# Kernel tuning notes

Measured on AMD Instinct MI355X. Metric: run time of the kernel, lower is better.

## Reference

```python
import jax, jax.numpy as jnp
import numpy as np

DECAY = 0.999
EPS = 1e-05
COMMITMENT_COST = 0.25
M, D = 1024, 256
B, H, W = 32, 32, 32


def setup_inputs() -> dict:
    key = jax.random.key(0)
    k1, k2 = jax.random.split(key)
    init_bound = 1.0 / M
    x = jax.random.normal(k1, (B, H, W, D), dtype=jnp.float32)
    embedding = jax.random.uniform(k2, (M, D), dtype=jnp.float32,
                                   minval=-init_bound, maxval=init_bound)
    ema_count = jnp.zeros((M,), dtype=jnp.float32)
    ema_weight = embedding  # buffer initialized as embedding.clone()
    return {"x": x, "embedding": embedding, "ema_count": ema_count,
            "ema_weight": ema_weight}


def reference(x, embedding, ema_count, ema_weight):
    Mn, Dn = embedding.shape
    x_flat = jax.lax.stop_gradient(x).reshape(-1, Dn)          # [N, D]
    N = x_flat.shape[0]

    # (-cdist)^2 == squared euclidean distance; argmin is the same.
    x_sq = jnp.sum(x_flat * x_flat, axis=-1, keepdims=True)    # [N, 1]
    e_sq = jnp.sum(embedding * embedding, axis=-1)             # [M]
    distances = x_sq - 2.0 * (x_flat @ embedding.T) + e_sq[None, :]  # [N, M]
    indices = jnp.argmin(distances, axis=-1)                   # [N]

    quantized = embedding[indices].reshape(x.shape)            # gather

    # one-hot column sums == scatter-add of ones; encodings.T @ x_flat == scatter-add rows
    counts = jnp.zeros((Mn,), x.dtype).at[indices].add(1.0)    # [M]
    dw = jnp.zeros((Mn, Dn), x.dtype).at[indices].add(x_flat)  # [M, D]

    new_count = DECAY * ema_count + (1.0 - DECAY) * counts
    n = jnp.sum(new_count)
    new_count = (new_count + EPS) / (n + Mn * EPS) * n
    new_weight = DECAY * ema_weight + (1.0 - DECAY) * dw
    new_embedding = new_weight / new_count[:, None]

    codebook_loss = jnp.mean((jax.lax.stop_gradient(x) - quantized) ** 2)
    e_latent_loss = jnp.mean((x - jax.lax.stop_gradient(quantized)) ** 2)
    commitment_loss = COMMITMENT_COST * e_latent_loss

    quantized_st = x + jax.lax.stop_gradient(quantized - x)    # straight-through

    avg_probs = counts / N
    perplexity = jnp.exp(-jnp.sum(avg_probs * jnp.log(avg_probs + 1e-10)))

    return (quantized_st, commitment_loss, codebook_loss, perplexity,
            new_embedding, new_count, new_weight)
```

## Files before the change

kernel.cpp:

```cpp
#include <hip/hip_runtime.h>
#include <cfloat>
#include <math.h>

#define N_TOK 32768
#define DIM   256
#define MCODE 1024

typedef unsigned short u16;
typedef unsigned long long u64;
typedef __attribute__((ext_vector_type(8))) _Float16 h16x8;
typedef __attribute__((ext_vector_type(4))) float f32x4;

constexpr float DECAY_ = 0.999f;
constexpr float OMD_   = (float)(1.0 - 0.999);
constexpr float EPS_   = 1e-5f;
constexpr float MEPS_  = (float)(1024 * 1e-5);

constexpr int WS_EH   = 0;
constexpr int WS_EL   = 131072;
constexpr int WS_ESQ  = 262144;
constexpr int WS_CNTI = 263168;
constexpr int WS_BI   = 264192;
constexpr int WS_LP   = 296960;
constexpr int WS_KEY  = 299008;

constexpr int OUT_Q        = 0;
constexpr int OUT_COMMIT   = 8388608;
constexpr int OUT_CODEBOOK = 8388609;
constexpr int OUT_PERP     = 8388610;
constexpr int OUT_NE       = 8388611;
constexpr int OUT_NC       = 8650755;
constexpr int OUT_NW       = 8651779;

static __device__ __forceinline__ void gl2lds16(const u16* g, char* l) {
    __builtin_amdgcn_global_load_lds(
        (const __attribute__((address_space(1))) unsigned int*)g,
        (__attribute__((address_space(3))) unsigned int*)l, 16, 0, 0);
}
static __device__ __forceinline__ unsigned fmap(float f) {
    unsigned u = __float_as_uint(f);
    return (u & 0x80000000u) ? ~u : (u | 0x80000000u);
}

static __device__ __forceinline__ void load_row8(const float* __restrict__ src,
                                                 int wave_id, int lane,
                                                 float* vv, size_t* o) {
    int rb = wave_id >> 6, kc = (wave_id >> 3) & 7, t = wave_id & 7;
    int row = rb * 128 + t * 16 + (lane & 15);
    int k   = kc * 32 + (lane >> 4) * 8;
    const float* s = &src[row * DIM + k];
    float4 v0 = *(const float4*)s, v1 = *(const float4*)(s + 4);
    vv[0]=v0.x; vv[1]=v0.y; vv[2]=v0.z; vv[3]=v0.w;
    vv[4]=v1.x; vv[5]=v1.y; vv[6]=v1.z; vv[7]=v1.w;
    *o = (size_t)wave_id * 512 + lane * 8;
}
static __device__ __forceinline__ void pack_wave_h16(const float* __restrict__ src,
                                                     u16* __restrict__ dst,
                                                     int wave_id, int lane,
                                                     float scale) {
    float vv[8]; size_t o;
    load_row8(src, wave_id, lane, vv, &o);
    h16x8 hv;
#pragma unroll
    for (int j = 0; j < 8; ++j) hv[j] = (_Float16)(vv[j] * scale);
    *(h16x8*)&dst[o] = hv;
}

__global__ __launch_bounds__(256) void vq_setup(const float* __restrict__ x,
                                                const float* __restrict__ emb,
                                                u16* __restrict__ xh,
                                                u16* __restrict__ eh,
                                                float* __restrict__ esq,
                                                u64* __restrict__ keys,
                                                int* __restrict__ cnti) {
    const int b = blockIdx.x, tid = threadIdx.x;
    const int lane = tid & 63, w = tid >> 6;
    if (b < 4096) { pack_wave_h16(x, xh, b * 4 + w, lane, 1.0f); return; }
    const int p = b - 4096;
    if (p < 128) {
        pack_wave_h16(emb, eh, p * 4 + w, lane, 1024.0f);
    } else if (p < 384) {
        int c = (p - 128) * 4 + w;
        float4 v = *(const float4*)&emb[c * DIM + lane * 4];
        float s = v.x * v.x + v.y * v.y + v.z * v.z + v.w * v.w;
#pragma unroll
        for (int off = 32; off; off >>= 1) s += __shfl_xor(s, off, 64);
        if (lane == 0) esq[c] = s;
    } else if (p < 512) {
        keys[(p - 384) * 256 + tid] = ~0ULL;
    } else {
#pragma unroll
        for (int i = 0; i < 4; ++i) cnti[i * 256 + tid] = 0;
    }
}

__global__ __launch_bounds__(256) void vq_scores_mfma(const u16* __restrict__ xh,
                                                      const u16* __restrict__ eh,
                                                      const float* __restrict__ esq,
                                                      u64* __restrict__ keys) {
    __shared__ __align__(16) char smem[33792];
    const int tid  = threadIdx.x;
    const int lane = tid & 63, w = tid >> 6;
    const int wm = w & 1, wn = w >> 1;
    const int raw = blockIdx.x;
    const int rb = (raw >> 6) * 8 + (raw & 7);
    const int cs = (raw >> 3) & 7;

    const u16* gb0 = xh + (size_t)rb * 32768;
    const u16* gb1 = eh + (size_t)cs * 32768;

    const h16x8* Ah = (const h16x8*)(smem);
    const h16x8* Bh = (const h16x8*)(smem + 8192);

    f32x4 acc[4][4];
#pragma unroll
    for (int i = 0; i < 4; ++i)
#pragma unroll
        for (int j = 0; j < 4; ++j) acc[i][j] = (f32x4)0.f;

    for (int kc = 0; kc < 8; ++kc) {
        __syncthreads();
#pragma unroll
        for (int j = 0; j < 4; ++j) {
            int t = w * 4 + j;
            int arr = t >> 3, slot = t & 7;
            const u16* g = (arr == 0 ? gb0 : gb1)
                           + kc * 4096 + slot * 512 + lane * 8;
            gl2lds16(g, smem + arr * 8192 + slot * 1024);
        }
        __syncthreads();

        h16x8 ah[4];
#pragma unroll
        for (int tm = 0; tm < 4; ++tm)
            ah[tm] = Ah[(wm * 4 + tm) * 64 + lane];
#pragma unroll
        for (int tn = 0; tn < 4; ++tn) {
            h16x8 bh = Bh[(wn * 4 + tn) * 64 + lane];
#pragma unroll
            for (int tm = 0; tm < 4; ++tm) {
                acc[tm][tn] = __builtin_amdgcn_mfma_f32_16x16x32_f16(ah[tm], bh, acc[tm][tn], 0, 0, 0);
            }
        }
    }

    __syncthreads();
    float* cv = (float*)smem;
    int*   ci = (int*)(smem + 16896);
    const int ln = lane & 15, quad = lane >> 4;
#pragma unroll
    for (int tm = 0; tm < 4; ++tm) {
        float bv[4];
        int   bi[4];
#pragma unroll
        for (int r = 0; r < 4; ++r) { bv[r] = FLT_MAX; bi[r] = 0; }
#pragma unroll
        for (int tn = 0; tn < 4; ++tn) {
            int c = cs * 128 + wn * 64 + tn * 16 + ln;
            float ec = esq[c];
#pragma unroll
            for (int r = 0; r < 4; ++r) {
                float d = fmaf(-0.001953125f, acc[tm][tn][r], ec);
                if (d < bv[r]) { bv[r] = d; bi[r] = c; }
            }
        }
        int row0 = wm * 64 + tm * 16 + quad * 4;
        int slot = wn * 16 + ln;
#pragma unroll
        for (int r = 0; r < 4; ++r) {
            cv[(row0 + r) * 33 + slot] = bv[r];
            ci[(row0 + r) * 33 + slot] = bi[r];
        }
    }
    __syncthreads();
    if (tid < 128) {
        float bv = cv[tid * 33];
        int   bi = ci[tid * 33];
#pragma unroll
        for (int s = 1; s < 32; ++s) {
            float v = cv[tid * 33 + s];
            int  ix = ci[tid * 33 + s];
            if (v < bv || (v == bv && ix < bi)) { bv = v; bi = ix; }
        }
        u64 key = ((u64)fmap(bv) << 32) | (unsigned)bi;
        atomicMin(&keys[rb * 128 + tid], key);
    }
}

__global__ __launch_bounds__(256) void vq_quant(const float* __restrict__ x,
                                                const float* __restrict__ emb,
                                                const u64* __restrict__ keys,
                                                float* __restrict__ outq,
                                                int* __restrict__ cnti,
                                                int* __restrict__ bi_arr,
                                                float* __restrict__ lpart) {
    const int tid = threadIdx.x, lane = tid & 63, w = tid >> 6;
    const float4* x4 = (const float4*)x;
    const float4* e4 = (const float4*)emb;
    float4* o4 = (float4*)outq;
    float lacc = 0.f;
#pragma unroll
    for (int it = 0; it < 4; ++it) {
        int row = blockIdx.x * 16 + it * 4 + w;
        int bi = (int)(unsigned)(keys[row] & 0xffffffffULL);
        if (lane == 0) { atomicAdd(&cnti[bi], 1); bi_arr[row] = bi; }
        float4 xv = x4[row * 64 + lane];
        float4 ev = e4[bi * 64 + lane];
        float4 q;
        q.x = xv.x + (ev.x - xv.x);  q.y = xv.y + (ev.y - xv.y);
        q.z = xv.z + (ev.z - xv.z);  q.w = xv.w + (ev.w - xv.w);
        o4[row * 64 + lane] = q;
        float dx = xv.x - ev.x, dy = xv.y - ev.y, dz = xv.z - ev.z, dwv = xv.w - ev.w;
        lacc += dx * dx + dy * dy + dz * dz + dwv * dwv;
    }
#pragma unroll
    for (int off = 32; off; off >>= 1) lacc += __shfl_xor(lacc, off, 64);
    __shared__ float red[4];
    if (lane == 0) red[w] = lacc;
    __syncthreads();
    if (tid == 0) lpart[blockIdx.x] = red[0] + red[1] + red[2] + red[3];
}

#define MEGA_CAP 6144
__global__ __launch_bounds__(256) void vq_mega(const float* __restrict__ x,
                                               const float* __restrict__ ema_count,
                                               const float* __restrict__ ema_weight,
                                               const int* __restrict__ cnti,
                                               const int* __restrict__ bi_arr,
                                               const float* __restrict__ lpart,
                                               float* __restrict__ out) {
    const int m = blockIdx.x, tid = threadIdx.x;
    __shared__ float fs[256];
    __shared__ int list[MEGA_CAP];
    __shared__ int lcount;

    float rsum = 0.f;
#pragma unroll
    for (int i = 0; i < 4; ++i) rsum += ema_count[tid * 4 + i];
    fs[tid] = rsum;
    if (tid == 0) lcount = 0;
    __syncthreads();
    for (int s = 128; s; s >>= 1) { if (tid < s) fs[tid] += fs[tid + s]; __syncthreads(); }
    const float n = DECAY_ * fs[0] + OMD_ * (float)N_TOK;
    __syncthreads();

    const int4* b4 = (const int4*)bi_arr;
#pragma unroll 4
    for (int i = tid; i < N_TOK / 4; i += 256) {
        int4 v = b4[i];
        if (v.x == m) { int p = atomicAdd(&lcount, 1); if (p < MEGA_CAP) list[p] = 4 * i; }
        if (v.y == m) { int p = atomicAdd(&lcount, 1); if (p < MEGA_CAP) list[p] = 4 * i + 1; }
        if (v.z == m) { int p = atomicAdd(&lcount, 1); if (p < MEGA_CAP) list[p] = 4 * i + 2; }
        if (v.w == m) { int p = atomicAdd(&lcount, 1); if (p < MEGA_CAP) list[p] = 4 * i + 3; }
    }
    __syncthreads();
    const int nm = lcount;
    float dwsum;
    if (nm <= MEGA_CAP) {
        float a0 = 0.f, a1 = 0.f, a2 = 0.f, a3 = 0.f;
        int i = 0;
        for (; i + 4 <= nm; i += 4) {
            a0 += x[list[i]     * DIM + tid];
            a1 += x[list[i + 1] * DIM + tid];
            a2 += x[list[i + 2] * DIM + tid];
            a3 += x[list[i + 3] * DIM + tid];
        }
        for (; i < nm; ++i) a0 += x[list[i] * DIM + tid];
        dwsum = (a0 + a1) + (a2 + a3);
    } else {
        __shared__ int chunk[256];
        float a0 = 0.f;
        for (int base = 0; base < N_TOK; base += 256) {
            __syncthreads();
            chunk[tid] = bi_arr[base + tid];
            __syncthreads();
            for (int j = 0; j < 256; ++j)
                if (chunk[j] == m) a0 += x[(base + j) * DIM + tid];
        }
        dwsum = a0;
    }

    float raw_m = DECAY_ * ema_count[m] + OMD_ * (float)nm;
    float ncm = (raw_m + EPS_) / (n + MEPS_) * n;
    float nw = DECAY_ * ema_weight[m * DIM + tid] + OMD_ * dwsum;
    out[OUT_NW + m * DIM + tid] = nw;
    out[OUT_NE + m * DIM + tid] = nw / ncm;
    if (tid == 0) out[OUT_NC + m] = ncm;

    if (m == 0) {
        float ent = 0.f;
#pragma unroll
        for (int i = 0; i < 4; ++i) {
            float p = (float)cnti[tid * 4 + i] / (float)N_TOK;
            ent += p * logf(p + 1e-10f);
        }
        __syncthreads();
        fs[tid] = ent;
        __syncthreads();
        for (int s = 128; s; s >>= 1) { if (tid < s) fs[tid] += fs[tid + s]; __syncthreads(); }
        float entr = fs[0];
        __syncthreads();
        float ls = 0.f;
#pragma unroll
        for (int k = 0; k < 8; ++k) ls += lpart[tid + 256 * k];
        fs[tid] = ls;
        __syncthreads();
        for (int s = 128; s; s >>= 1) { if (tid < s) fs[tid] += fs[tid + s]; __syncthreads(); }
        if (tid == 0) {
            float mean = fs[0] / (float)(N_TOK * DIM);
            out[OUT_COMMIT]   = 0.25f * mean;
            out[OUT_CODEBOOK] = mean;
            out[OUT_PERP]     = expf(-entr);
        }
    }
}

extern "C" void kernel_launch(void* const* d_in, const int* in_sizes, int n_in,
                              void* d_out, int out_size, void* d_ws, size_t ws_size,
                              hipStream_t stream) {
    const float* x          = (const float*)d_in[0];
    const float* emb        = (const float*)d_in[1];
    const float* ema_count  = (const float*)d_in[2];
    const float* ema_weight = (const float*)d_in[3];
    float* out = (float*)d_out;
    float* wf  = (float*)d_ws;

    u16* xh = (u16*)d_out;
    u16* eh = (u16*)(wf + WS_EH);

    float* esq    = wf + WS_ESQ;
    int*   cnti   = (int*)(wf + WS_CNTI);
    int*   bi_arr = (int*)(wf + WS_BI);
    float* lpart  = wf + WS_LP;
    u64*   keys   = (u64*)(wf + WS_KEY);

    vq_setup<<<4609, 256, 0, stream>>>(x, emb, xh, eh, esq, keys, cnti);
    vq_scores_mfma<<<2048, 256, 0, stream>>>(xh, eh, esq, keys);
    vq_quant<<<2048, 256, 0, stream>>>(x, emb, keys, out, cnti, bi_arr, lpart);
    vq_mega<<<MCODE, 256, 0, stream>>>(x, ema_count, ema_weight, cnti, bi_arr,
                                       lpart, out);
}
```

Baseline: 149.8 us.

## Fold quantize/loss pass into per-code EMA kernel and drop vq_quant

Removes the separate vq_quant kernel and has each per-code block in vq_mega write the straight-through quantized rows, accumulate the squared-error loss, and compute its entropy term directly from the argmin keys. Global loss and perplexity are finished by the last block through float atomics and a completion counter. This saves one launch and one full pass over x and the output. In exchange, the quantized writes become scattered 1-float-per-thread row stores, the keys scan reads twice as many bytes, and the float atomic sums make the loss nondeterministic.

```diff
diff --git a/kernel.cpp b/kernel.cpp
--- a/kernel.cpp
+++ b/kernel.cpp
@@ -17,11 +17,8 @@
 constexpr float MEPS_  = (float)(1024 * 1e-5);
 
 constexpr int WS_EH   = 0;
-constexpr int WS_EL   = 131072;
 constexpr int WS_ESQ  = 262144;
-constexpr int WS_CNTI = 263168;
-constexpr int WS_BI   = 264192;
-constexpr int WS_LP   = 296960;
+constexpr int WS_SCAL = 263168;
 constexpr int WS_KEY  = 299008;
 
 constexpr int OUT_Q        = 0;
@@ -72,7 +69,7 @@
                                                 u16* __restrict__ eh,
                                                 float* __restrict__ esq,
                                                 u64* __restrict__ keys,
-                                                int* __restrict__ cnti) {
+                                                float* __restrict__ scal) {
     const int b = blockIdx.x, tid = threadIdx.x;
     const int lane = tid & 63, w = tid >> 6;
     if (b < 4096) { pack_wave_h16(x, xh, b * 4 + w, lane, 1.0f); return; }
@@ -89,8 +86,7 @@
     } else if (p < 512) {
         keys[(p - 384) * 256 + tid] = ~0ULL;
     } else {
-#pragma unroll
-        for (int i = 0; i < 4; ++i) cnti[i * 256 + tid] = 0;
+        if (tid < 4) scal[tid] = 0.f;
     }
 }
 
@@ -187,48 +183,14 @@
     }
 }
 
-__global__ __launch_bounds__(256) void vq_quant(const float* __restrict__ x,
-                                                const float* __restrict__ emb,
-                                                const u64* __restrict__ keys,
-                                                float* __restrict__ outq,
-                                                int* __restrict__ cnti,
-                                                int* __restrict__ bi_arr,
-                                                float* __restrict__ lpart) {
-    const int tid = threadIdx.x, lane = tid & 63, w = tid >> 6;
-    const float4* x4 = (const float4*)x;
-    const float4* e4 = (const float4*)emb;
-    float4* o4 = (float4*)outq;
-    float lacc = 0.f;
-#pragma unroll
-    for (int it = 0; it < 4; ++it) {
-        int row = blockIdx.x * 16 + it * 4 + w;
-        int bi = (int)(unsigned)(keys[row] & 0xffffffffULL);
-        if (lane == 0) { atomicAdd(&cnti[bi], 1); bi_arr[row] = bi; }
-        float4 xv = x4[row * 64 + lane];
-        float4 ev = e4[bi * 64 + lane];
-        float4 q;
-        q.x = xv.x + (ev.x - xv.x);  q.y = xv.y + (ev.y - xv.y);
-        q.z = xv.z + (ev.z - xv.z);  q.w = xv.w + (ev.w - xv.w);
-        o4[row * 64 + lane] = q;
-        float dx = xv.x - ev.x, dy = xv.y - ev.y, dz = xv.z - ev.z, dwv = xv.w - ev.w;
-        lacc += dx * dx + dy * dy + dz * dz + dwv * dwv;
-    }
-#pragma unroll
-    for (int off = 32; off; off >>= 1) lacc += __shfl_xor(lacc, off, 64);
-    __shared__ float red[4];
-    if (lane == 0) red[w] = lacc;
-    __syncthreads();
-    if (tid == 0) lpart[blockIdx.x] = red[0] + red[1] + red[2] + red[3];
-}
-
 #define MEGA_CAP 6144
 __global__ __launch_bounds__(256) void vq_mega(const float* __restrict__ x,
+                                               const float* __restrict__ emb,
                                                const float* __restrict__ ema_count,
                                                const float* __restrict__ ema_weight,
-                                               const int* __restrict__ cnti,
-                                               const int* __restrict__ bi_arr,
-                                               const float* __restrict__ lpart,
-                                               float* __restrict__ out) {
+                                               const u64* __restrict__ keys,
+                                               float* __restrict__ out,
+                                               float* __restrict__ scal) {
     const int m = blockIdx.x, tid = threadIdx.x;
     __shared__ float fs[256];
     __shared__ int list[MEGA_CAP];
@@ -244,38 +206,59 @@
     const float n = DECAY_ * fs[0] + OMD_ * (float)N_TOK;
     __syncthreads();
 
-    const int4* b4 = (const int4*)bi_arr;
+    const float ev = emb[m * DIM + tid];
+
+    const int4* k4 = (const int4*)keys;
 #pragma unroll 4
-    for (int i = tid; i < N_TOK / 4; i += 256) {
-        int4 v = b4[i];
-        if (v.x == m) { int p = atomicAdd(&lcount, 1); if (p < MEGA_CAP) list[p] = 4 * i; }
-        if (v.y == m) { int p = atomicAdd(&lcount, 1); if (p < MEGA_CAP) list[p] = 4 * i + 1; }
-        if (v.z == m) { int p = atomicAdd(&lcount, 1); if (p < MEGA_CAP) list[p] = 4 * i + 2; }
-        if (v.w == m) { int p = atomicAdd(&lcount, 1); if (p < MEGA_CAP) list[p] = 4 * i + 3; }
+    for (int i = tid; i < N_TOK / 2; i += 256) {
+        int4 v = k4[i];
+        if (v.x == m) { int p = atomicAdd(&lcount, 1); if (p < MEGA_CAP) list[p] = 2 * i; }
+        if (v.z == m) { int p = atomicAdd(&lcount, 1); if (p < MEGA_CAP) list[p] = 2 * i + 1; }
     }
     __syncthreads();
     const int nm = lcount;
+    float lacc = 0.f;
     float dwsum;
     if (nm <= MEGA_CAP) {
         float a0 = 0.f, a1 = 0.f, a2 = 0.f, a3 = 0.f;
         int i = 0;
         for (; i + 4 <= nm; i += 4) {
-            a0 += x[list[i]     * DIM + tid];
-            a1 += x[list[i + 1] * DIM + tid];
-            a2 += x[list[i + 2] * DIM + tid];
-            a3 += x[list[i + 3] * DIM + tid];
-        }
-        for (; i < nm; ++i) a0 += x[list[i] * DIM + tid];
+            int r0 = list[i], r1 = list[i + 1], r2 = list[i + 2], r3 = list[i + 3];
+            float x0 = x[r0 * DIM + tid];
+            float x1 = x[r1 * DIM + tid];
+            float x2 = x[r2 * DIM + tid];
+            float x3 = x[r3 * DIM + tid];
+            out[OUT_Q + r0 * DIM + tid] = x0 + (ev - x0);
+            out[OUT_Q + r1 * DIM + tid] = x1 + (ev - x1);
+            out[OUT_Q + r2 * DIM + tid] = x2 + (ev - x2);
+            out[OUT_Q + r3 * DIM + tid] = x3 + (ev - x3);
+            float d0 = x0 - ev, d1 = x1 - ev, d2 = x2 - ev, d3 = x3 - ev;
+            lacc += d0 * d0 + d1 * d1 + d2 * d2 + d3 * d3;
+            a0 += x0; a1 += x1; a2 += x2; a3 += x3;
+        }
+        for (; i < nm; ++i) {
+            int r = list[i];
+            float xv = x[r * DIM + tid];
+            out[OUT_Q + r * DIM + tid] = xv + (ev - xv);
+            float d = xv - ev; lacc += d * d;
+            a0 += xv;
+        }
         dwsum = (a0 + a1) + (a2 + a3);
     } else {
         __shared__ int chunk[256];
         float a0 = 0.f;
         for (int base = 0; base < N_TOK; base += 256) {
             __syncthreads();
-            chunk[tid] = bi_arr[base + tid];
+            chunk[tid] = (int)(unsigned)(keys[base + tid] & 0xffffffffULL);
             __syncthreads();
             for (int j = 0; j < 256; ++j)
-                if (chunk[j] == m) a0 += x[(base + j) * DIM + tid];
+                if (chunk[j] == m) {
+                    int r = base + j;
+                    float xv = x[r * DIM + tid];
+                    out[OUT_Q + r * DIM + tid] = xv + (ev - xv);
+                    float d = xv - ev; lacc += d * d;
+                    a0 += xv;
+                }
         }
         dwsum = a0;
     }
@@ -287,30 +270,24 @@
     out[OUT_NE + m * DIM + tid] = nw / ncm;
     if (tid == 0) out[OUT_NC + m] = ncm;
 
-    if (m == 0) {
-        float ent = 0.f;
-#pragma unroll
-        for (int i = 0; i < 4; ++i) {
-            float p = (float)cnti[tid * 4 + i] / (float)N_TOK;
-            ent += p * logf(p + 1e-10f);
-        }
-        __syncthreads();
-        fs[tid] = ent;
-        __syncthreads();
-        for (int s = 128; s; s >>= 1) { if (tid < s) fs[tid] += fs[tid + s]; __syncthreads(); }
-        float entr = fs[0];
-        __syncthreads();
-        float ls = 0.f;
-#pragma unroll
-        for (int k = 0; k < 8; ++k) ls += lpart[tid + 256 * k];
-        fs[tid] = ls;
-        __syncthreads();
-        for (int s = 128; s; s >>= 1) { if (tid < s) fs[tid] += fs[tid + s]; __syncthreads(); }
-        if (tid == 0) {
-            float mean = fs[0] / (float)(N_TOK * DIM);
+    __syncthreads();
+    fs[tid] = lacc;
+    __syncthreads();
+    for (int s = 128; s; s >>= 1) { if (tid < s) fs[tid] += fs[tid + s]; __syncthreads(); }
+    if (tid == 0) {
+        atomicAdd(&scal[0], fs[0]);
+        float p = (float)nm / (float)N_TOK;
+        atomicAdd(&scal[1], p * logf(p + 1e-10f));
+        __threadfence();
+        int prev = atomicAdd((int*)&scal[2], 1);
+        if (prev == MCODE - 1) {
+            __threadfence();
+            float ls = atomicAdd(&scal[0], 0.0f);
+            float es = atomicAdd(&scal[1], 0.0f);
+            float mean = ls / (float)(N_TOK * DIM);
             out[OUT_COMMIT]   = 0.25f * mean;
             out[OUT_CODEBOOK] = mean;
-            out[OUT_PERP]     = expf(-entr);
+            out[OUT_PERP]     = expf(-es);
         }
     }
 }
@@ -328,15 +305,12 @@
     u16* xh = (u16*)d_out;
     u16* eh = (u16*)(wf + WS_EH);
 
-    float* esq    = wf + WS_ESQ;
-    int*   cnti   = (int*)(wf + WS_CNTI);
-    int*   bi_arr = (int*)(wf + WS_BI);
-    float* lpart  = wf + WS_LP;
-    u64*   keys   = (u64*)(wf + WS_KEY);
-
-    vq_setup<<<4609, 256, 0, stream>>>(x, emb, xh, eh, esq, keys, cnti);
+    float* esq  = wf + WS_ESQ;
+    float* scal = wf + WS_SCAL;
+    u64*   keys = (u64*)(wf + WS_KEY);
+
+    vq_setup<<<4609, 256, 0, stream>>>(x, emb, xh, eh, esq, keys, scal);
     vq_scores_mfma<<<2048, 256, 0, stream>>>(xh, eh, esq, keys);
-    vq_quant<<<2048, 256, 0, stream>>>(x, emb, keys, out, cnti, bi_arr, lpart);
-    vq_mega<<<MCODE, 256, 0, stream>>>(x, ema_count, ema_weight, cnti, bi_arr,
-                                       lpart, out);
-}
+    vq_mega<<<MCODE, 256, 0, stream>>>(x, emb, ema_count, ema_weight, keys,
+                                       out, scal);
+}
```

New measurement: 191.1 us. +27.6%, slower.
